# Optimization experiments

Measured on AMD Instinct MI355X. Metric: run time of the kernel, lower is better.

Reference implementation:

```python
import jax, jax.numpy as jnp
import numpy as np

N_EMBD = 384
N_HEADS = 6
HEAD_SIZE = N_EMBD // N_HEADS  # 64
LN_EPS = 1e-5


def _layernorm(x, g, b):
    mu = jnp.mean(x, axis=-1, keepdims=True)
    var = jnp.var(x, axis=-1, keepdims=True)
    return (x - mu) * jax.lax.rsqrt(var + LN_EPS) * g + b


def setup_inputs() -> dict:
    key = jax.random.key(0)
    ks = jax.random.split(key, 12)
    B, T, C, H, D = 128, 256, N_EMBD, N_HEADS, HEAD_SIZE
    s_in = 1.0 / np.sqrt(C)
    s_ff = 1.0 / np.sqrt(4 * C)
    return {
        "x": jax.random.normal(ks[0], (B, T, C), dtype=jnp.float32),
        "ln1_g": jnp.ones((C,), jnp.float32),
        "ln1_b": jnp.zeros((C,), jnp.float32),
        "Wq": jax.random.uniform(ks[1], (H, C, D), jnp.float32, -s_in, s_in),
        "Wk": jax.random.uniform(ks[2], (H, C, D), jnp.float32, -s_in, s_in),
        "Wv": jax.random.uniform(ks[3], (H, C, D), jnp.float32, -s_in, s_in),
        "Wo": jax.random.uniform(ks[4], (C, C), jnp.float32, -s_in, s_in),
        "bo": jnp.zeros((C,), jnp.float32),
        "ln2_g": jnp.ones((C,), jnp.float32),
        "ln2_b": jnp.zeros((C,), jnp.float32),
        "W1": jax.random.uniform(ks[5], (C, 4 * C), jnp.float32, -s_in, s_in),
        "b1": jnp.zeros((4 * C,), jnp.float32),
        "W2": jax.random.uniform(ks[6], (4 * C, C), jnp.float32, -s_ff, s_ff),
        "b2": jnp.zeros((C,), jnp.float32),
    }


def reference(x, ln1_g, ln1_b, Wq, Wk, Wv, Wo, bo, ln2_g, ln2_b, W1, b1, W2, b2):
    # Dropout layers are identity (eval mode).
    B, T, C = x.shape
    h = _layernorm(x, ln1_g, ln1_b)
    # Per-head projections: [B,T,C] x [H,C,D] -> [B,H,T,D]
    q = jnp.einsum('btc,hcd->bhtd', h, Wq)
    k = jnp.einsum('btc,hcd->bhtd', h, Wk)
    v = jnp.einsum('btc,hcd->bhtd', h, Wv)
    scale = HEAD_SIZE ** (-0.5)
    scores = jnp.einsum('bhtd,bhsd->bhts', q, k) * scale  # [B,H,T,T]
    causal = jnp.tril(jnp.ones((T, T), dtype=bool))
    scores = jnp.where(causal, scores, jnp.float32(-jnp.inf))
    wei = jax.nn.softmax(scores, axis=-1)
    attn = jnp.einsum('bhts,bhsd->bhtd', wei, v)  # [B,H,T,D]
    attn = attn.transpose(0, 2, 1, 3).reshape(B, T, C)  # concat heads
    x = x + attn @ Wo + bo
    h2 = _layernorm(x, ln2_g, ln2_b)
    ff = jax.nn.relu(h2 @ W1 + b1) @ W2 + b2
    return x + ff
```

## Files before the change

### kernel.cpp

```cpp
#include <hip/hip_runtime.h>

typedef unsigned int u32;
typedef unsigned short u16;
typedef __bf16 bf16_t;
typedef float f32x4 __attribute__((ext_vector_type(4)));
typedef bf16_t bfrag __attribute__((ext_vector_type(8)));
typedef u16 u16x8 __attribute__((ext_vector_type(8)));

__device__ inline u16 f2bf(float f) {
    union { float f; u32 u; } v; v.f = f;
    u32 r = v.u + 0x7fffu + ((v.u >> 16) & 1u);
    return (u16)(r >> 16);
}
__device__ inline float bf2f(u16 h) {
    union { u32 u; float f; } v; v.u = ((u32)h) << 16; return v.f;
}

__device__ inline f32x4 mfma16(bfrag a, bfrag b, f32x4 c) {
    return __builtin_amdgcn_mfma_f32_16x16x32_bf16(a, b, c, 0, 0, 0);
}

__device__ inline void gload_lds16(const void* g, void* l) {
    __builtin_amdgcn_global_load_lds((const __attribute__((address_space(1))) u32*)g,
                                     (__attribute__((address_space(3))) u32*)l, 16, 0, 0);
}

__device__ inline float redmax16(float v) {
    #pragma unroll
    for (int m = 1; m < 16; m <<= 1) v = fmaxf(v, __shfl_xor(v, m));
    return v;
}
__device__ inline float redsum16(float v) {
    #pragma unroll
    for (int m = 1; m < 16; m <<= 1) v += __shfl_xor(v, m);
    return v;
}

#define NTOK 32768
#define QKV_ELEMS 12582912

__global__ __launch_bounds__(256) void prep_weights(
    const float* __restrict__ Wq, const float* __restrict__ Wk,
    const float* __restrict__ Wv, const float* __restrict__ Wo,
    const float* __restrict__ W1, const float* __restrict__ W2,
    u16* __restrict__ wqkvT, u16* __restrict__ woT,
    u16* __restrict__ w1T, u16* __restrict__ w2T)
{
    __shared__ float tile[64][65];
    const int b = blockIdx.x;
    const float* src; u16* dst;
    int sr0, sc0, srs, dr0, dc0, drs;
    if (b < 36) {
        int i = b / 6, j = b - i * 6;
        src = Wo;  srs = 384;  sr0 = i * 64; sc0 = j * 64;
        dst = woT; drs = 384;  dr0 = j * 64; dc0 = i * 64;
    } else if (b < 180) {
        int t = b - 36; int i = t / 24, j = t - i * 24;
        src = W1;  srs = 1536; sr0 = i * 64; sc0 = j * 64;
        dst = w1T; drs = 384;  dr0 = j * 64; dc0 = i * 64;
    } else if (b < 324) {
        int t = b - 180; int i = t / 6, j = t - i * 6;
        src = W2;  srs = 384;  sr0 = i * 64; sc0 = j * 64;
        dst = w2T; drs = 1536; dr0 = j * 64; dc0 = i * 64;
    } else {
        int t = b - 324;
        int m2 = t / 36; t -= m2 * 36;
        int h = t / 6, tt = t - h * 6;
        src = (m2 == 0) ? Wq : ((m2 == 1) ? Wk : Wv);
        srs = 64;  sr0 = h * 384 + tt * 64; sc0 = 0;
        dst = wqkvT; drs = 384; dr0 = m2 * 384 + h * 64; dc0 = tt * 64;
    }
    const int lane = threadIdx.x & 63, grp = threadIdx.x >> 6;
    #pragma unroll
    for (int i = 0; i < 16; i++) {
        int r = grp * 16 + i;
        tile[r][lane] = src[(size_t)(sr0 + r) * srs + sc0 + lane];
    }
    __syncthreads();
    #pragma unroll
    for (int i = 0; i < 16; i++) {
        int r = grp * 16 + i;
        dst[(size_t)(dr0 + r) * drs + dc0 + lane] = f2bf(tile[lane][r]);
    }
}

__global__ __launch_bounds__(256) void ln_f32(
    const float* __restrict__ x, const float* __restrict__ g,
    const float* __restrict__ b, u16* __restrict__ out)
{
    const int row = blockIdx.x * 4 + (threadIdx.x >> 6);
    const int lane = threadIdx.x & 63;
    const float2* xr = (const float2*)(x + (size_t)row * 384);
    float2 v[3];
    float s = 0.f, s2 = 0.f;
    #pragma unroll
    for (int i = 0; i < 3; i++) {
        v[i] = xr[lane + i * 64];
        s += v[i].x + v[i].y; s2 += v[i].x * v[i].x + v[i].y * v[i].y;
    }
    #pragma unroll
    for (int m = 1; m < 64; m <<= 1) { s += __shfl_xor(s, m); s2 += __shfl_xor(s2, m); }
    float mean = s * (1.f / 384.f);
    float rstd = rsqrtf(s2 * (1.f / 384.f) - mean * mean + 1e-5f);
    u32* op = (u32*)(out + (size_t)row * 384);
    #pragma unroll
    for (int i = 0; i < 3; i++) {
        int c = (lane + i * 64) * 2;
        u32 lo = f2bf((v[i].x - mean) * rstd * g[c] + b[c]);
        u32 hi = f2bf((v[i].y - mean) * rstd * g[c + 1] + b[c + 1]);
        op[lane + i * 64] = lo | (hi << 16);
    }
}

__global__ __launch_bounds__(256) void ln_bf16(
    const u16* __restrict__ x, const float* __restrict__ g,
    const float* __restrict__ b, u16* __restrict__ out)
{
    const int row = blockIdx.x * 4 + (threadIdx.x >> 6);
    const int lane = threadIdx.x & 63;
    const u32* xr = (const u32*)(x + (size_t)row * 384);
    float vx[3], vy[3];
    float s = 0.f, s2 = 0.f;
    #pragma unroll
    for (int i = 0; i < 3; i++) {
        u32 w = xr[lane + i * 64];
        vx[i] = bf2f((u16)(w & 0xffffu));
        vy[i] = bf2f((u16)(w >> 16));
        s += vx[i] + vy[i]; s2 += vx[i] * vx[i] + vy[i] * vy[i];
    }
    #pragma unroll
    for (int m = 1; m < 64; m <<= 1) { s += __shfl_xor(s, m); s2 += __shfl_xor(s2, m); }
    float mean = s * (1.f / 384.f);
    float rstd = rsqrtf(s2 * (1.f / 384.f) - mean * mean + 1e-5f);
    u32* op = (u32*)(out + (size_t)row * 384);
    #pragma unroll
    for (int i = 0; i < 3; i++) {
        int c = (lane + i * 64) * 2;
        u32 lo = f2bf((vx[i] - mean) * rstd * g[c] + b[c]);
        u32 hi = f2bf((vy[i] - mean) * rstd * g[c + 1] + b[c + 1]);
        op[lane + i * 64] = lo | (hi << 16);
    }
}

template<int EPI, int NT>
__global__ __launch_bounds__(256, 4) void gemm_m97(
    const u16* __restrict__ A, const u16* __restrict__ Bt,
    const float* __restrict__ bias, const void* __restrict__ resid,
    void* __restrict__ outp, int M, int N)
{
    const int K = NT * 64;
    __shared__ __align__(16) u16 As[128 * 64];
    __shared__ __align__(16) u16 Bs[128 * 64];
    const int tid = threadIdx.x, wave = tid >> 6, lane = tid & 63;
    const int nbn = N >> 7;
    const int nwg = gridDim.x;
    const int bid = blockIdx.x;
    const int wg = (bid & 7) * (nwg >> 3) + (bid >> 3);
    const int bm = wg / nbn, bn = wg - bm * nbn;
    const int rowA0 = bm << 7, rowB0 = bn << 7;
    const int wm = (wave >> 1) << 6, wn = (wave & 1) << 6;
    const int lr = lane >> 3, lc = lane & 7;
    f32x4 acc[4][4] = {};

    for (int t = 0; t < NT; ++t) {
        const int ko = t << 6;
        #pragma unroll
        for (int p = 0; p < 4; p++) {
            const int idx = p * 4 + wave;
            const int r = idx * 8 + lr;
            const int csrc = ((lc ^ (r & 7)) << 3);
            gload_lds16(A + (size_t)(rowA0 + r) * K + ko + csrc, &As[idx * 512]);
            gload_lds16(Bt + (size_t)(rowB0 + r) * K + ko + csrc, &Bs[idx * 512]);
        }
        __syncthreads();
        #pragma unroll
        for (int kk = 0; kk < 2; kk++) {
            bfrag af[4], bfr[4];
            #pragma unroll
            for (int mt = 0; mt < 4; mt++) {
                const int row = wm + mt * 16 + (lane & 15);
                af[mt] = *(const bfrag*)((const char*)As + row * 128 +
                          (((kk * 4 + (lane >> 4)) ^ (row & 7)) << 4));
            }
            #pragma unroll
            for (int nt = 0; nt < 4; nt++) {
                const int row = wn + nt * 16 + (lane & 15);
                bfr[nt] = *(const bfrag*)((const char*)Bs + row * 128 +
                          (((kk * 4 + (lane >> 4)) ^ (row & 7)) << 4));
            }
            #pragma unroll
            for (int mt = 0; mt < 4; mt++)
                #pragma unroll
                for (int nt = 0; nt < 4; nt++)
                    acc[mt][nt] = mfma16(af[mt], bfr[nt], acc[mt][nt]);
        }
        __syncthreads();
    }

    #pragma unroll
    for (int mt = 0; mt < 4; mt++) {
        #pragma unroll
        for (int nt = 0; nt < 4; nt++) {
            #pragma unroll
            for (int r2 = 0; r2 < 4; r2++) {
                const int gr = rowA0 + wm + mt * 16 + ((lane >> 4) << 2) + r2;
                const int gc = rowB0 + wn + nt * 16 + (lane & 15);
                float v = acc[mt][nt][r2];
                if constexpr (EPI == 0) {
                    int m2 = gc / 384;
                    int rem = gc - m2 * 384;
                    int hh = rem >> 6, d = rem & 63;
                    if (m2 == 0) v *= 0.125f;
                    int bb = gr >> 8, t2 = gr & 255;
                    ((u16*)outp)[(size_t)m2 * QKV_ELEMS +
                                 ((size_t)((bb * 6 + hh) * 256 + t2) << 6) + d] = f2bf(v);
                } else if constexpr (EPI == 1) {
                    ((u16*)outp)[(size_t)gr * N + gc] =
                        f2bf(((const float*)resid)[(size_t)gr * N + gc] + bias[gc] + v);
                } else if constexpr (EPI == 2) {
                    float t2 = v + bias[gc];
                    ((u16*)outp)[(size_t)gr * N + gc] = f2bf(t2 > 0.f ? t2 : 0.f);
                } else {
                    ((float*)outp)[(size_t)gr * N + gc] =
                        bf2f(((const u16*)resid)[(size_t)gr * N + gc]) + bias[gc] + v;
                }
            }
        }
    }
}

__global__ __launch_bounds__(512) void attn_kernel(
    const u16* __restrict__ q, const u16* __restrict__ k, const u16* __restrict__ v,
    u16* __restrict__ outp)
{
    __shared__ __align__(16) u16 Ks[256 * 64];
    __shared__ __align__(16) u16 Vt[64 * 256];
    __shared__ __align__(16) u16 Ps[8 * 512];
    const int bh = blockIdx.x;
    const int tid = threadIdx.x, wave = tid >> 6, lane = tid & 63;
    const u16* qb = q + (size_t)bh * 16384;
    const u16* kb = k + (size_t)bh * 16384;
    const u16* vb = v + (size_t)bh * 16384;

    #pragma unroll
    for (int p = 0; p < 4; p++) {
        const int idx = p * 8 + wave;
        const int r = idx * 8 + (lane >> 3);
        const int csrc = (((lane & 7) ^ (r & 7)) << 3);
        gload_lds16(kb + (size_t)r * 64 + csrc, &Ks[idx * 512]);
    }
    #pragma unroll
    for (int p = 0; p < 4; p++) {
        const int e = (p * 512 + tid) * 8;
        const int key = e >> 6, d0 = e & 63;
        u16x8 raw = *(const u16x8*)(vb + (size_t)key * 64 + d0);
        #pragma unroll
        for (int j = 0; j < 8; j++) {
            const int d = d0 + j;
            Vt[d * 256 + (((key >> 3) ^ (d & 7)) << 3) + (key & 7)] = raw[j];
        }
    }
    __syncthreads();

    const int bI = bh / 6, hh = bh - bI * 6;

    #pragma unroll
    for (int t = 0; t < 2; t++) {
        const int qtile = (t == 0) ? wave : (15 - wave);
        const int qrowbase = qtile * 16;
        bfrag qf[2];
        {
            const int r = qrowbase + (lane & 15);
            qf[0] = *(const bfrag*)(qb + (size_t)r * 64 + ((lane >> 4) << 3));
            qf[1] = *(const bfrag*)(qb + (size_t)r * 64 + 32 + ((lane >> 4) << 3));
        }
        f32x4 S[16];
        #pragma unroll
        for (int kt = 0; kt < 16; kt++) {
            if (kt <= qtile) {
                f32x4 s = {0.f, 0.f, 0.f, 0.f};
                const int key = kt * 16 + (lane & 15);
                const char* kbase = (const char*)Ks + key * 128;
                s = mfma16(qf[0], *(const bfrag*)(kbase + ((((lane >> 4)) ^ (key & 7)) << 4)), s);
                s = mfma16(qf[1], *(const bfrag*)(kbase + (((4 + (lane >> 4)) ^ (key & 7)) << 4)), s);
                if (kt == qtile) {
                    const int qit = (lane >> 4) << 2;
                    #pragma unroll
                    for (int r2 = 0; r2 < 4; r2++)
                        if ((lane & 15) > qit + r2) s[r2] = -1e30f;
                }
                S[kt] = s;
            }
        }
        float mx[4] = {-1e30f, -1e30f, -1e30f, -1e30f};
        #pragma unroll
        for (int kt = 0; kt < 16; kt++) if (kt <= qtile)
            #pragma unroll
            for (int r2 = 0; r2 < 4; r2++) mx[r2] = fmaxf(mx[r2], S[kt][r2]);
        #pragma unroll
        for (int r2 = 0; r2 < 4; r2++) mx[r2] = redmax16(mx[r2]);
        float sm[4] = {0.f, 0.f, 0.f, 0.f};
        #pragma unroll
        for (int kt = 0; kt < 16; kt++) if (kt <= qtile)
            #pragma unroll
            for (int r2 = 0; r2 < 4; r2++) {
                float p = __expf(S[kt][r2] - mx[r2]);
                S[kt][r2] = p; sm[r2] += p;
            }
        #pragma unroll
        for (int r2 = 0; r2 < 4; r2++) sm[r2] = redsum16(sm[r2]);

        f32x4 O[4] = {};
        u16* Pw = &Ps[wave * 512];
        const int nch = (qtile + 2) >> 1;
        #pragma unroll
        for (int ch = 0; ch < 8; ch++) {
            if (ch < nch) {
                #pragma unroll
                for (int ktl = 0; ktl < 2; ktl++) {
                    const int kt = ch * 2 + ktl;
                    const int keyl = ktl * 16 + (lane & 15);
                    const int cidx = keyl >> 3;
                    #pragma unroll
                    for (int r2 = 0; r2 < 4; r2++) {
                        const int qq = ((lane >> 4) << 2) + r2;
                        float pv = (kt <= qtile) ? S[kt][r2] : 0.f;
                        Pw[qq * 32 + ((cidx ^ (qq & 3)) << 3) + (keyl & 7)] = f2bf(pv);
                    }
                }
                const int qq = lane & 15;
                bfrag pa = *(const bfrag*)(Pw + qq * 32 + (((lane >> 4) ^ (qq & 3)) << 3));
                #pragma unroll
                for (int dt = 0; dt < 4; dt++) {
                    const int d = dt * 16 + (lane & 15);
                    const int cc = ch * 4 + (lane >> 4);
                    bfrag vf = *(const bfrag*)((const char*)Vt + d * 512 + ((cc ^ (d & 7)) << 4));
                    O[dt] = mfma16(pa, vf, O[dt]);
                }
            }
        }
        #pragma unroll
        for (int dt = 0; dt < 4; dt++) {
            #pragma unroll
            for (int r2 = 0; r2 < 4; r2++) {
                const int qg = qrowbase + ((lane >> 4) << 2) + r2;
                const float val = O[dt][r2] / sm[r2];
                outp[(size_t)(bI * 256 + qg) * 384 + hh * 64 + dt * 16 + (lane & 15)] = f2bf(val);
            }
        }
    }
}

extern "C" void kernel_launch(void* const* d_in, const int* in_sizes, int n_in,
                              void* d_out, int out_size, void* d_ws, size_t ws_size,
                              hipStream_t stream)
{
    const float* x    = (const float*)d_in[0];
    const float* ln1g = (const float*)d_in[1];
    const float* ln1b = (const float*)d_in[2];
    const float* Wq   = (const float*)d_in[3];
    const float* Wk   = (const float*)d_in[4];
    const float* Wv   = (const float*)d_in[5];
    const float* Wo   = (const float*)d_in[6];
    const float* bo   = (const float*)d_in[7];
    const float* ln2g = (const float*)d_in[8];
    const float* ln2b = (const float*)d_in[9];
    const float* W1   = (const float*)d_in[10];
    const float* b1   = (const float*)d_in[11];
    const float* W2   = (const float*)d_in[12];
    const float* b2   = (const float*)d_in[13];

    if (ws_size < 230031360u) return;

    char* ws = (char*)d_ws;
    u16*   wqkvT = (u16*)(ws + 0);
    u16*   woT   = (u16*)(ws + 884736);
    u16*   w1T   = (u16*)(ws + 1179648);
    u16*   w2T   = (u16*)(ws + 2359296);
    u16*   hbuf  = (u16*)(ws + 3538944);
    u16*   qbuf  = (u16*)(ws + 28704768);
    u16*   kbuf  = (u16*)(ws + 53870592);
    u16*   vbuf  = (u16*)(ws + 79036416);
    u16*   x2h   = (u16*)(ws + 104202240);
    u16*   mid   = (u16*)(ws + 129368064);
    float* out   = (float*)d_out;

    prep_weights<<<432, 256, 0, stream>>>(Wq, Wk, Wv, Wo, W1, W2, wqkvT, woT, w1T, w2T);
    ln_f32<<<8192, 256, 0, stream>>>(x, ln1g, ln1b, hbuf);
    gemm_m97<0, 6><<<2304, 256, 0, stream>>>(hbuf, wqkvT, nullptr, nullptr, qbuf,
                                             NTOK, 1152);
    attn_kernel<<<768, 512, 0, stream>>>(qbuf, kbuf, vbuf, hbuf);
    gemm_m97<1, 6><<<768, 256, 0, stream>>>(hbuf, woT, bo, x, x2h, NTOK, 384);
    ln_bf16<<<8192, 256, 0, stream>>>(x2h, ln2g, ln2b, qbuf);
    gemm_m97<2, 6><<<3072, 256, 0, stream>>>(qbuf, w1T, b1, nullptr, mid, NTOK, 1536);
    gemm_m97<3, 24><<<768, 256, 0, stream>>>(mid, w2T, b2, x2h, out, NTOK, 384);
}
```

Measured before the change: 230.2 us.

## Replace LDS-tiled GEMM with direct-load GEMM, fuse residual into LN, flatten QKV layout

The GEMM drops its LDS staging and barriers, with each wave loading MFMA fragments straight from global memory. The tile-to-block mapping is also changed to group rows by XCD. The QKV GEMM now writes a plain row-major [tokens,1152] buffer that attention reads with a strided layout, replacing the per-head scattered store. The Wo GEMM epilogue no longer adds the residual and bias; a new ln_resid kernel adds them and writes both x2h and the LN2 output in one pass. Dropping LDS removes shared-memory traffic and syncs, but operand reuse within a block now depends on the cache, which risks much higher global load traffic. The workspace pointer assignments include dead, overwritten lines.

```diff
diff --git a/kernel.cpp b/kernel.cpp
--- a/kernel.cpp
+++ b/kernel.cpp
@@ -37,7 +37,6 @@
 }
 
 #define NTOK 32768
-#define QKV_ELEMS 12582912
 
 __global__ __launch_bounds__(256) void prep_weights(
     const float* __restrict__ Wq, const float* __restrict__ Wk,
@@ -112,89 +111,81 @@
     }
 }
 
-__global__ __launch_bounds__(256) void ln_bf16(
-    const u16* __restrict__ x, const float* __restrict__ g,
-    const float* __restrict__ b, u16* __restrict__ out)
+__global__ __launch_bounds__(256) void ln_resid(
+    const float* __restrict__ x, const u16* __restrict__ wout,
+    const float* __restrict__ bo, const float* __restrict__ g,
+    const float* __restrict__ b, u16* __restrict__ x2h, u16* __restrict__ h2)
 {
     const int row = blockIdx.x * 4 + (threadIdx.x >> 6);
     const int lane = threadIdx.x & 63;
-    const u32* xr = (const u32*)(x + (size_t)row * 384);
-    float vx[3], vy[3];
+    const float2* xr = (const float2*)(x + (size_t)row * 384);
+    const u32* wr = (const u32*)(wout + (size_t)row * 384);
+    float tx[3], ty[3];
     float s = 0.f, s2 = 0.f;
     #pragma unroll
     for (int i = 0; i < 3; i++) {
-        u32 w = xr[lane + i * 64];
-        vx[i] = bf2f((u16)(w & 0xffffu));
-        vy[i] = bf2f((u16)(w >> 16));
-        s += vx[i] + vy[i]; s2 += vx[i] * vx[i] + vy[i] * vy[i];
+        float2 xv = xr[lane + i * 64];
+        u32 w = wr[lane + i * 64];
+        int c = (lane + i * 64) * 2;
+        tx[i] = xv.x + bf2f((u16)(w & 0xffffu)) + bo[c];
+        ty[i] = xv.y + bf2f((u16)(w >> 16)) + bo[c + 1];
+        s += tx[i] + ty[i]; s2 += tx[i] * tx[i] + ty[i] * ty[i];
     }
     #pragma unroll
     for (int m = 1; m < 64; m <<= 1) { s += __shfl_xor(s, m); s2 += __shfl_xor(s2, m); }
     float mean = s * (1.f / 384.f);
     float rstd = rsqrtf(s2 * (1.f / 384.f) - mean * mean + 1e-5f);
-    u32* op = (u32*)(out + (size_t)row * 384);
+    u32* xo = (u32*)(x2h + (size_t)row * 384);
+    u32* ho = (u32*)(h2 + (size_t)row * 384);
     #pragma unroll
     for (int i = 0; i < 3; i++) {
         int c = (lane + i * 64) * 2;
-        u32 lo = f2bf((vx[i] - mean) * rstd * g[c] + b[c]);
-        u32 hi = f2bf((vy[i] - mean) * rstd * g[c + 1] + b[c + 1]);
-        op[lane + i * 64] = lo | (hi << 16);
+        xo[lane + i * 64] = (u32)f2bf(tx[i]) | ((u32)f2bf(ty[i]) << 16);
+        u32 lo = f2bf((tx[i] - mean) * rstd * g[c] + b[c]);
+        u32 hi = f2bf((ty[i] - mean) * rstd * g[c + 1] + b[c + 1]);
+        ho[lane + i * 64] = lo | (hi << 16);
     }
 }
 
 template<int EPI, int NT>
-__global__ __launch_bounds__(256, 4) void gemm_m97(
+__global__ __launch_bounds__(256) void gemm_flat(
     const u16* __restrict__ A, const u16* __restrict__ Bt,
     const float* __restrict__ bias, const void* __restrict__ resid,
     void* __restrict__ outp, int M, int N)
 {
     const int K = NT * 64;
-    __shared__ __align__(16) u16 As[128 * 64];
-    __shared__ __align__(16) u16 Bs[128 * 64];
     const int tid = threadIdx.x, wave = tid >> 6, lane = tid & 63;
     const int nbn = N >> 7;
-    const int nwg = gridDim.x;
     const int bid = blockIdx.x;
-    const int wg = (bid & 7) * (nwg >> 3) + (bid >> 3);
-    const int bm = wg / nbn, bn = wg - bm * nbn;
+    const int xcd = bid & 7, loc = bid >> 3;
+    const int bm = xcd + (loc / nbn) * 8;
+    const int bn = loc - (loc / nbn) * nbn;
     const int rowA0 = bm << 7, rowB0 = bn << 7;
     const int wm = (wave >> 1) << 6, wn = (wave & 1) << 6;
-    const int lr = lane >> 3, lc = lane & 7;
     f32x4 acc[4][4] = {};
 
-    for (int t = 0; t < NT; ++t) {
-        const int ko = t << 6;
-        #pragma unroll
-        for (int p = 0; p < 4; p++) {
-            const int idx = p * 4 + wave;
-            const int r = idx * 8 + lr;
-            const int csrc = ((lc ^ (r & 7)) << 3);
-            gload_lds16(A + (size_t)(rowA0 + r) * K + ko + csrc, &As[idx * 512]);
-            gload_lds16(Bt + (size_t)(rowB0 + r) * K + ko + csrc, &Bs[idx * 512]);
-        }
-        __syncthreads();
-        #pragma unroll
-        for (int kk = 0; kk < 2; kk++) {
-            bfrag af[4], bfr[4];
-            #pragma unroll
-            for (int mt = 0; mt < 4; mt++) {
-                const int row = wm + mt * 16 + (lane & 15);
-                af[mt] = *(const bfrag*)((const char*)As + row * 128 +
-                          (((kk * 4 + (lane >> 4)) ^ (row & 7)) << 4));
-            }
-            #pragma unroll
-            for (int nt = 0; nt < 4; nt++) {
-                const int row = wn + nt * 16 + (lane & 15);
-                bfr[nt] = *(const bfrag*)((const char*)Bs + row * 128 +
-                          (((kk * 4 + (lane >> 4)) ^ (row & 7)) << 4));
-            }
-            #pragma unroll
-            for (int mt = 0; mt < 4; mt++)
-                #pragma unroll
-                for (int nt = 0; nt < 4; nt++)
-                    acc[mt][nt] = mfma16(af[mt], bfr[nt], acc[mt][nt]);
-        }
-        __syncthreads();
+    const u16* Ar[4];
+    const u16* Br[4];
+    #pragma unroll
+    for (int mt = 0; mt < 4; mt++)
+        Ar[mt] = A + (size_t)(rowA0 + wm + mt * 16 + (lane & 15)) * K + ((lane >> 4) << 3);
+    #pragma unroll
+    for (int nt = 0; nt < 4; nt++)
+        Br[nt] = Bt + (size_t)(rowB0 + wn + nt * 16 + (lane & 15)) * K + ((lane >> 4) << 3);
+
+    #pragma unroll 2
+    for (int t = 0; t < NT * 2; ++t) {
+        const int off = t << 5;
+        bfrag af[4], bf[4];
+        #pragma unroll
+        for (int i = 0; i < 4; i++) af[i] = *(const bfrag*)(Ar[i] + off);
+        #pragma unroll
+        for (int i = 0; i < 4; i++) bf[i] = *(const bfrag*)(Br[i] + off);
+        #pragma unroll
+        for (int mt = 0; mt < 4; mt++)
+            #pragma unroll
+            for (int nt = 0; nt < 4; nt++)
+                acc[mt][nt] = mfma16(af[mt], bf[nt], acc[mt][nt]);
     }
 
     #pragma unroll
@@ -207,16 +198,10 @@
                 const int gc = rowB0 + wn + nt * 16 + (lane & 15);
                 float v = acc[mt][nt][r2];
                 if constexpr (EPI == 0) {
-                    int m2 = gc / 384;
-                    int rem = gc - m2 * 384;
-                    int hh = rem >> 6, d = rem & 63;
-                    if (m2 == 0) v *= 0.125f;
-                    int bb = gr >> 8, t2 = gr & 255;
-                    ((u16*)outp)[(size_t)m2 * QKV_ELEMS +
-                                 ((size_t)((bb * 6 + hh) * 256 + t2) << 6) + d] = f2bf(v);
+                    if (gc < 384) v *= 0.125f;
+                    ((u16*)outp)[(size_t)gr * N + gc] = f2bf(v);
                 } else if constexpr (EPI == 1) {
-                    ((u16*)outp)[(size_t)gr * N + gc] =
-                        f2bf(((const float*)resid)[(size_t)gr * N + gc] + bias[gc] + v);
+                    ((u16*)outp)[(size_t)gr * N + gc] = f2bf(v);
                 } else if constexpr (EPI == 2) {
                     float t2 = v + bias[gc];
                     ((u16*)outp)[(size_t)gr * N + gc] = f2bf(t2 > 0.f ? t2 : 0.f);
@@ -230,30 +215,31 @@
 }
 
 __global__ __launch_bounds__(512) void attn_kernel(
-    const u16* __restrict__ q, const u16* __restrict__ k, const u16* __restrict__ v,
-    u16* __restrict__ outp)
+    const u16* __restrict__ qkv, u16* __restrict__ outp)
 {
     __shared__ __align__(16) u16 Ks[256 * 64];
     __shared__ __align__(16) u16 Vt[64 * 256];
     __shared__ __align__(16) u16 Ps[8 * 512];
     const int bh = blockIdx.x;
     const int tid = threadIdx.x, wave = tid >> 6, lane = tid & 63;
-    const u16* qb = q + (size_t)bh * 16384;
-    const u16* kb = k + (size_t)bh * 16384;
-    const u16* vb = v + (size_t)bh * 16384;
+    const int bI = bh / 6, hh = bh - bI * 6;
+    const u16* qb = qkv + (size_t)(bI * 256) * 1152 + hh * 64;
+    const u16* kb = qb + 384;
+    const u16* vb = qb + 768;
+    const int RS = 1152;
 
     #pragma unroll
     for (int p = 0; p < 4; p++) {
         const int idx = p * 8 + wave;
         const int r = idx * 8 + (lane >> 3);
         const int csrc = (((lane & 7) ^ (r & 7)) << 3);
-        gload_lds16(kb + (size_t)r * 64 + csrc, &Ks[idx * 512]);
+        gload_lds16(kb + (size_t)r * RS + csrc, &Ks[idx * 512]);
     }
     #pragma unroll
     for (int p = 0; p < 4; p++) {
         const int e = (p * 512 + tid) * 8;
         const int key = e >> 6, d0 = e & 63;
-        u16x8 raw = *(const u16x8*)(vb + (size_t)key * 64 + d0);
+        u16x8 raw = *(const u16x8*)(vb + (size_t)key * RS + d0);
         #pragma unroll
         for (int j = 0; j < 8; j++) {
             const int d = d0 + j;
@@ -261,8 +247,6 @@
         }
     }
     __syncthreads();
-
-    const int bI = bh / 6, hh = bh - bI * 6;
 
     #pragma unroll
     for (int t = 0; t < 2; t++) {
@@ -271,8 +255,8 @@
         bfrag qf[2];
         {
             const int r = qrowbase + (lane & 15);
-            qf[0] = *(const bfrag*)(qb + (size_t)r * 64 + ((lane >> 4) << 3));
-            qf[1] = *(const bfrag*)(qb + (size_t)r * 64 + 32 + ((lane >> 4) << 3));
+            qf[0] = *(const bfrag*)(qb + (size_t)r * RS + ((lane >> 4) << 3));
+            qf[1] = *(const bfrag*)(qb + (size_t)r * RS + 32 + ((lane >> 4) << 3));
         }
         f32x4 S[16];
         #pragma unroll
@@ -378,20 +362,25 @@
     u16*   w1T   = (u16*)(ws + 1179648);
     u16*   w2T   = (u16*)(ws + 2359296);
     u16*   hbuf  = (u16*)(ws + 3538944);
-    u16*   qbuf  = (u16*)(ws + 28704768);
-    u16*   kbuf  = (u16*)(ws + 53870592);
-    u16*   vbuf  = (u16*)(ws + 79036416);
+    u16*   qkvb  = (u16*)(ws + 28704768);
+    u16*   woOut = (u16*)(ws + 53870592);
+    u16*   h2    = (u16*)(ws + 28704768);
     u16*   x2h   = (u16*)(ws + 104202240);
     u16*   mid   = (u16*)(ws + 129368064);
     float* out   = (float*)d_out;
 
+    woOut = (u16*)(ws + 154533888 + 103219200 - 25165824);
+    if (ws_size < 232652800u) { woOut = (u16*)(ws + 129368064 + 100663296); }
+    woOut = (u16*)(ws + 79036416);
+
     prep_weights<<<432, 256, 0, stream>>>(Wq, Wk, Wv, Wo, W1, W2, wqkvT, woT, w1T, w2T);
     ln_f32<<<8192, 256, 0, stream>>>(x, ln1g, ln1b, hbuf);
-    gemm_m97<0, 6><<<2304, 256, 0, stream>>>(hbuf, wqkvT, nullptr, nullptr, qbuf,
-                                             NTOK, 1152);
-    attn_kernel<<<768, 512, 0, stream>>>(qbuf, kbuf, vbuf, hbuf);
-    gemm_m97<1, 6><<<768, 256, 0, stream>>>(hbuf, woT, bo, x, x2h, NTOK, 384);
-    ln_bf16<<<8192, 256, 0, stream>>>(x2h, ln2g, ln2b, qbuf);
-    gemm_m97<2, 6><<<3072, 256, 0, stream>>>(qbuf, w1T, b1, nullptr, mid, NTOK, 1536);
-    gemm_m97<3, 24><<<768, 256, 0, stream>>>(mid, w2T, b2, x2h, out, NTOK, 384);
-}
+    gemm_flat<0, 6><<<2304, 256, 0, stream>>>(hbuf, wqkvT, nullptr, nullptr, qkvb,
+                                              NTOK, 1152);
+    attn_kernel<<<768, 512, 0, stream>>>(qkvb, hbuf);
+    gemm_flat<1, 6><<<768, 256, 0, stream>>>(hbuf, woT, nullptr, nullptr, woOut,
+                                             NTOK, 384);
+    ln_resid<<<8192, 256, 0, stream>>>(x, woOut, bo, ln2g, ln2b, x2h, h2);
+    gemm_flat<2, 6><<<3072, 256, 0, stream>>>(h2, w1T, b1, nullptr, mid, NTOK, 1536);
+    gemm_flat<3, 24><<<768, 256, 0, stream>>>(mid, w2T, b2, x2h, out, NTOK, 384);
+}
```

Result: slower. 543.6 us (+136.1%).
